# Optimization experiments

Measured on AMD Instinct MI355X. Metric: run time of the kernel, lower is better.

Reference implementation:

```python
import jax, jax.numpy as jnp
import numpy as np
from jax import lax

B, C, W = 16, 64, 125000  # batch, EEG channels, raw samples
KH, KW, SW, OC = 3, 2500, 1250, 32


def setup_inputs() -> dict:
    key = jax.random.key(0)
    ks = jax.random.split(key, 10)
    inp = {
        "x": jax.random.normal(ks[0], (B, 1, C, W), dtype=jnp.float32),
        # Conv2d(1->32, kernel=(3,2500))
        "conv_w": jax.random.normal(ks[1], (OC, 1, KH, KW), dtype=jnp.float32) * 0.02,
        "conv_b": jax.random.normal(ks[2], (OC,), dtype=jnp.float32) * 0.02,
        # Conv2d(32->1, kernel=(1,1))
        "conv2_w": jax.random.normal(ks[3], (1, OC, 1, 1), dtype=jnp.float32) * 0.1,
        "conv2_b": jax.random.normal(ks[4], (1,), dtype=jnp.float32) * 0.1,
        # nn.RNN(input_size=1, hidden_size=1): scalar weights
        "w_ih": jax.random.normal(ks[5], (1, 1), dtype=jnp.float32),
        "w_hh": jax.random.normal(ks[6], (1, 1), dtype=jnp.float32),
        "b_ih": jax.random.normal(ks[7], (1,), dtype=jnp.float32) * 0.1,
        "b_hh": jax.random.normal(ks[8], (1,), dtype=jnp.float32) * 0.1,
        # torch.rand(num_layers=1, B, 1) hidden init, reused for every row i
        "h0": jax.random.uniform(ks[9], (1, B, 1), dtype=jnp.float32),
    }
    return inp


def reference(x, conv_w, conv_b, conv2_w, conv2_b, w_ih, w_hh, b_ih, b_hh, h0):
    # F.pad(x, (0,0,1,1), 'replicate'): pad channel (height) dim by 1 each side
    xp = jnp.pad(x, ((0, 0), (0, 0), (1, 1), (0, 0)), mode="edge")
    # conv + relu -> [B, 32, C, T]
    y = lax.conv_general_dilated(
        xp, conv_w, window_strides=(1, SW), padding="VALID",
        dimension_numbers=("NCHW", "OIHW", "NCHW"))
    y = jax.nn.relu(y + conv_b[None, :, None, None])
    # 1x1 conv 32->1 + relu -> [B, C, T]
    z = jnp.einsum("bohw,o->bhw", y, conv2_w[0, :, 0, 0]) + conv2_b[0]
    z = jax.nn.relu(z)
    # Elman RNN with scalar weights, scanned over T; carry is [B, C]
    wih, whh = w_ih[0, 0], w_hh[0, 0]
    bias = b_ih[0] + b_hh[0]
    h_init = jnp.broadcast_to(h0[0, :, 0][:, None], z.shape[:2])  # [B, C]

    def step(h, xt):  # xt: [B, C]
        h = jnp.tanh(wih * xt + whh * h + bias)
        return h, None

    xs = jnp.moveaxis(z, -1, 0)  # [T, B, C]
    h_final, _ = lax.scan(step, h_init, xs)
    return jax.nn.sigmoid(h_final)  # [B, C]
```

## Files before the change

### kernel.cpp

```cpp
#include <hip/hip_runtime.h>
#include <math.h>

#define B_ 16
#define C_ 64
#define T_ 99
#define KW_ 1250
#define KP_ 1280
#define N_ 192
#define M_ (B_*C_*100)
#define BM 32
#define NCHUNK 40

typedef __attribute__((ext_vector_type(8))) _Float16 half8;
typedef __attribute__((ext_vector_type(2))) _Float16 half2_t;
typedef __attribute__((ext_vector_type(4))) float f32x4;
typedef __attribute__((ext_vector_type(2), aligned(8))) float f32x2;

__global__ __launch_bounds__(256) void wconv_kernel(const float* __restrict__ cw,
                                                    _Float16* __restrict__ wh)
{
    int n = blockIdx.x;
    int o = n / 6, rem = n - o * 6, kh = rem >> 1, hf = rem & 1;
    const float* src = cw + o * 7500 + kh * 2500 + hf * 1250;
    for (int k = threadIdx.x; k < KP_; k += 256)
        wh[n * KP_ + k] = (k < KW_) ? (_Float16)src[k] : (_Float16)0.f;
}

__global__ __launch_bounds__(256, 2) void gemm_kernel(const float* __restrict__ x,
                                                      const _Float16* __restrict__ wh,
                                                      _Float16* __restrict__ P)
{
    __shared__ __align__(16) _Float16 smA[BM * KP_];

    const int tid  = threadIdx.x;
    const int bt   = blockIdx.x;
    const int lane = tid & 63;
    const int wave = tid >> 6;
    const int wn   = wave * 48;
    const int l15  = lane & 15;
    const int lq   = lane >> 4;
    const int l4   = lane >> 2;
    const int lm4  = lane & 3;

    {
        const float* xb = x + (size_t)(bt * BM + wave * 8) * KW_;
#pragma unroll
        for (int rr = 0; rr < 8; rr++) {
            const int row = wave * 8 + rr;
            const float* xr = xb + (size_t)rr * KW_;
            _Float16* drow = smA + row * KP_;
            const int r7 = row & 7;
#pragma unroll
            for (int s = 0; s < 10; s++) {
                int c = s * 128 + lane * 2;
                f32x2 v = (c <= KW_ - 2) ? *(const f32x2*)(xr + c)
                                         : (f32x2){0.f, 0.f};
                int blk = (s * 16 + l4) ^ r7;
                *(half2_t*)(drow + blk * 8 + lm4 * 2) =
                    (half2_t){(_Float16)v.x, (_Float16)v.y};
            }
        }
    }
    __syncthreads();

    const _Float16* bbase = wh + (size_t)(wn + l15) * KP_ + lq * 8;

    f32x4 acc[2][3];
#pragma unroll
    for (int mi = 0; mi < 2; mi++)
#pragma unroll
        for (int ni = 0; ni < 3; ni++) acc[mi][ni] = (f32x4){0.f, 0.f, 0.f, 0.f};

#pragma unroll 4
    for (int ck = 0; ck < NCHUNK; ck++) {
        half8 bfr[3];
#pragma unroll
        for (int ni = 0; ni < 3; ni++)
            bfr[ni] = *(const half8*)(bbase + (size_t)ni * 16 * KP_ + ck * 32);
        half8 afr[2];
#pragma unroll
        for (int mi = 0; mi < 2; mi++) {
            int row = mi * 16 + l15;
            int blk = (ck * 4 + lq) ^ (row & 7);
            afr[mi] = *(const half8*)(smA + row * KP_ + blk * 8);
        }
#pragma unroll
        for (int mi = 0; mi < 2; mi++)
#pragma unroll
            for (int ni = 0; ni < 3; ni++)
                acc[mi][ni] = __builtin_amdgcn_mfma_f32_16x16x32_f16(
                    afr[mi], bfr[ni], acc[mi][ni], 0, 0, 0);
    }

#pragma unroll
    for (int mi = 0; mi < 2; mi++) {
#pragma unroll
        for (int r2 = 0; r2 < 4; r2++) {
            int rloc = mi * 16 + lq * 4 + r2;
            int xr   = bt * BM + rloc;
            int bc   = xr / 100;
            int j    = xr - bc * 100;
            size_t mp = ((size_t)(bc >> 6) * 100 + j) * 64 + (bc & 63);
#pragma unroll
            for (int ni = 0; ni < 3; ni++) {
                int n = wn + ni * 16 + l15;
                P[mp * N_ + n] = (_Float16)acc[mi][ni][r2];
            }
        }
    }
}

__global__ __launch_bounds__(256) void combine_kernel(const _Float16* __restrict__ P,
                                                      const float* __restrict__ conv_b,
                                                      const float* __restrict__ c2w,
                                                      const float* __restrict__ c2b,
                                                      float* __restrict__ z)
{
    __shared__ float Pl[64][193];
    __shared__ float red[4][64];
    const int t   = blockIdx.x;
    const int b   = blockIdx.y;
    const int tid = threadIdx.x;
    const int c   = tid & 63;
    const int og  = tid >> 6;

    float v[8];
#pragma unroll
    for (int o = 0; o < 8; o++) v[o] = conv_b[og * 8 + o];

    for (int hf = 0; hf < 2; hf++) {
        const int j = t + hf;
        const _Float16* Pb = P + (size_t)((b * 100 + j) * 64) * N_;
        __syncthreads();
#pragma unroll
        for (int i = 0; i < 6; i++) {
            int e   = i * 256 + tid;
            half8 hdat = *(const half8*)(Pb + e * 8);
            int row = e / 24;
            int col = (e - row * 24) * 8;
#pragma unroll
            for (int u = 0; u < 8; u++) Pl[row][col + u] = (float)hdat[u];
        }
        __syncthreads();
#pragma unroll
        for (int kh = 0; kh < 3; kh++) {
            int r = c + kh - 1;
            r = r < 0 ? 0 : (r > 63 ? 63 : r);
#pragma unroll
            for (int o = 0; o < 8; o++)
                v[o] += Pl[r][(og * 8 + o) * 6 + kh * 2 + hf];
        }
    }

    float part = 0.f;
#pragma unroll
    for (int o = 0; o < 8; o++) part += fmaxf(v[o], 0.f) * c2w[og * 8 + o];
    red[og][c] = part;
    __syncthreads();
    if (og == 0) {
        float zz = red[0][c] + red[1][c] + red[2][c] + red[3][c] + c2b[0];
        z[t * (B_ * C_) + b * 64 + c] = fmaxf(zz, 0.f);
    }
}

__global__ __launch_bounds__(256) void rnn_kernel(const float* __restrict__ z,
                                                  const float* __restrict__ w_ih,
                                                  const float* __restrict__ w_hh,
                                                  const float* __restrict__ b_ih,
                                                  const float* __restrict__ b_hh,
                                                  const float* __restrict__ h0,
                                                  float* __restrict__ out)
{
    __shared__ float zs[50][256];
    const int tid = threadIdx.x;
    const int g   = blockIdx.x * 256 + tid;
    const int b   = g >> 6;
    const float wih  = w_ih[0];
    const float whh  = w_hh[0];
    const float bias = b_ih[0] + b_hh[0];
    float h = h0[b];
    for (int t0 = 0; t0 < T_; t0 += 50) {
        const int nt = (T_ - t0) < 50 ? (T_ - t0) : 50;
        __syncthreads();
        for (int tt = 0; tt < nt; tt++)
            zs[tt][tid] = z[(t0 + tt) * (B_ * C_) + g];
        __syncthreads();
        for (int tt = 0; tt < nt; tt++)
            h = tanhf(fmaf(wih, zs[tt][tid], fmaf(whh, h, bias)));
    }
    out[g] = 1.f / (1.f + expf(-h));
}

extern "C" void kernel_launch(void* const* d_in, const int* in_sizes, int n_in,
                              void* d_out, int out_size, void* d_ws, size_t ws_size,
                              hipStream_t stream)
{
    const float* x   = (const float*)d_in[0];
    const float* cw  = (const float*)d_in[1];
    const float* cb  = (const float*)d_in[2];
    const float* c2w = (const float*)d_in[3];
    const float* c2b = (const float*)d_in[4];
    const float* wih = (const float*)d_in[5];
    const float* whh = (const float*)d_in[6];
    const float* bih = (const float*)d_in[7];
    const float* bhh = (const float*)d_in[8];
    const float* h0  = (const float*)d_in[9];
    float* out = (float*)d_out;

    const size_t whbytes = (size_t)N_ * KP_ * sizeof(_Float16);
    const size_t pbytes  = (size_t)M_ * N_ * sizeof(_Float16);
    const size_t zbytes  = (size_t)B_ * C_ * T_ * sizeof(float);

    if (ws_size < whbytes + pbytes + zbytes) return;

    _Float16* wh = (_Float16*)d_ws;
    _Float16* P  = (_Float16*)((char*)d_ws + whbytes);
    float*    z  = (float*)((char*)d_ws + whbytes + pbytes);

    wconv_kernel<<<N_, 256, 0, stream>>>(cw, wh);
    gemm_kernel<<<M_ / BM, 256, 0, stream>>>(x, wh, P);
    combine_kernel<<<dim3(T_, B_), 256, 0, stream>>>(P, cb, c2w, c2b, z);
    rnn_kernel<<<4, 256, 0, stream>>>(z, wih, whh, bih, bhh, h0, out);
}
```

Before: 874.9 us.

## Double-buffer GEMM A tiles via async global-to-LDS loads with 64-row blocks

The GEMM kernel no longer converts each block's whole 32x1280 input tile to fp16 in shared memory before computing. It now streams 128-column fp32 slices of a 64-row tile straight into a double-buffered LDS area using global_load_lds, with explicit waitcnt and barriers. The fp32-to-fp16 conversion happens in registers when fragments are built, and the tail past column 1250 is zeroed by masking. Waves are arranged 2x2 with 6 N-fragments each, so loading the raw input overlaps with the MFMA work and the B fragments are reused more. In exchange it reads a little past row ends, including past the end of x for the final row, relies on possibly unaligned 16-byte LDS loads, and needs more accumulator registers.

```diff
diff --git a/kernel.cpp b/kernel.cpp
--- a/kernel.cpp
+++ b/kernel.cpp
@@ -8,13 +8,15 @@
 #define KP_ 1280
 #define N_ 192
 #define M_ (B_*C_*100)
-#define BM 32
-#define NCHUNK 40
+#define BM 64
+#define NSC 10
 
 typedef __attribute__((ext_vector_type(8))) _Float16 half8;
-typedef __attribute__((ext_vector_type(2))) _Float16 half2_t;
 typedef __attribute__((ext_vector_type(4))) float f32x4;
-typedef __attribute__((ext_vector_type(2), aligned(8))) float f32x2;
+
+#define GLD_LDS16(gp, lp) \
+    __builtin_amdgcn_global_load_lds((const __attribute__((address_space(1))) void*)(gp), \
+                                     (__attribute__((address_space(3))) void*)(lp), 16, 0, 0)
 
 __global__ __launch_bounds__(256) void wconv_kernel(const float* __restrict__ cw,
                                                     _Float16* __restrict__ wh)
@@ -30,79 +32,110 @@
                                                       const _Float16* __restrict__ wh,
                                                       _Float16* __restrict__ P)
 {
-    __shared__ __align__(16) _Float16 smA[BM * KP_];
+    __shared__ __align__(16) float smA[2][BM * 128];
 
     const int tid  = threadIdx.x;
     const int bt   = blockIdx.x;
     const int lane = tid & 63;
     const int wave = tid >> 6;
-    const int wn   = wave * 48;
+    const int wm   = (wave & 1) * 32;
+    const int wn   = (wave >> 1) * 96;
     const int l15  = lane & 15;
     const int lq   = lane >> 4;
-    const int l4   = lane >> 2;
-    const int lm4  = lane & 3;
-
-    {
-        const float* xb = x + (size_t)(bt * BM + wave * 8) * KW_;
-#pragma unroll
-        for (int rr = 0; rr < 8; rr++) {
-            const int row = wave * 8 + rr;
-            const float* xr = xb + (size_t)rr * KW_;
-            _Float16* drow = smA + row * KP_;
-            const int r7 = row & 7;
-#pragma unroll
-            for (int s = 0; s < 10; s++) {
-                int c = s * 128 + lane * 2;
-                f32x2 v = (c <= KW_ - 2) ? *(const f32x2*)(xr + c)
-                                         : (f32x2){0.f, 0.f};
-                int blk = (s * 16 + l4) ^ r7;
-                *(half2_t*)(drow + blk * 8 + lm4 * 2) =
-                    (half2_t){(_Float16)v.x, (_Float16)v.y};
+
+    const int ls = lane >> 5;
+    const int lb = lane & 31;
+    const float* xbase = x + (size_t)bt * BM * KW_;
+
+#define STAGE(sc_, buf_) do {                                                    \
+        _Pragma("unroll") for (int i_ = 0; i_ < 8; i_++) {                       \
+            const int q_   = wave * 8 + i_;                                      \
+            const int row_ = 2 * q_ + ls;                                        \
+            const int g_   = lb ^ (row_ & 7);                                    \
+            GLD_LDS16(xbase + (size_t)row_ * KW_ + (sc_) * 128 + g_ * 4,         \
+                      &smA[buf_][q_ * 256]);                                     \
+        }                                                                        \
+    } while (0)
+
+    const _Float16* bbase = wh + (size_t)(wn + l15) * KP_ + lq * 8;
+
+    f32x4 acc[2][6];
+#pragma unroll
+    for (int mi = 0; mi < 2; mi++)
+#pragma unroll
+        for (int ni = 0; ni < 6; ni++) acc[mi][ni] = (f32x4){0.f, 0.f, 0.f, 0.f};
+
+    STAGE(0, 0);
+    STAGE(1, 1);
+
+    for (int sc = 0; sc < NSC; sc++) {
+        const int buf = sc & 1;
+        const float* Ab = &smA[buf][0];
+        const bool tail = (sc == NSC - 1);
+
+        if (sc < NSC - 1) asm volatile("s_waitcnt vmcnt(8)" ::: "memory");
+        else              asm volatile("s_waitcnt vmcnt(0)" ::: "memory");
+        __builtin_amdgcn_s_barrier();
+        __builtin_amdgcn_sched_barrier(0);
+
+#pragma unroll
+        for (int ckl = 0; ckl < 4; ckl++) {
+            const int ck = sc * 4 + ckl;
+            half8 bfr[6];
+#pragma unroll
+            for (int ni = 0; ni < 6; ni++)
+                bfr[ni] = *(const half8*)(bbase + (size_t)ni * 16 * KP_ + ck * 32);
+
+            half8 afr[2];
+#pragma unroll
+            for (int mi = 0; mi < 2; mi++) {
+                const int row = wm + mi * 16 + l15;
+                const int r7  = row & 7;
+                const int b0  = ckl * 8 + lq * 2;
+                f32x4 lo = *(const f32x4*)(Ab + row * 128 + ((b0    ) ^ r7) * 4);
+                f32x4 hi = *(const f32x4*)(Ab + row * 128 + ((b0 + 1) ^ r7) * 4);
+                if (tail && ckl == 3) {
+                    if (lq != 0) {
+                        lo = (f32x4){0.f, 0.f, 0.f, 0.f};
+                        hi = (f32x4){0.f, 0.f, 0.f, 0.f};
+                    } else {
+                        lo[2] = 0.f; lo[3] = 0.f;
+                        hi = (f32x4){0.f, 0.f, 0.f, 0.f};
+                    }
+                }
+                half8 a;
+                a[0] = (_Float16)lo[0]; a[1] = (_Float16)lo[1];
+                a[2] = (_Float16)lo[2]; a[3] = (_Float16)lo[3];
+                a[4] = (_Float16)hi[0]; a[5] = (_Float16)hi[1];
+                a[6] = (_Float16)hi[2]; a[7] = (_Float16)hi[3];
+                afr[mi] = a;
             }
-        }
-    }
-    __syncthreads();
-
-    const _Float16* bbase = wh + (size_t)(wn + l15) * KP_ + lq * 8;
-
-    f32x4 acc[2][3];
-#pragma unroll
-    for (int mi = 0; mi < 2; mi++)
-#pragma unroll
-        for (int ni = 0; ni < 3; ni++) acc[mi][ni] = (f32x4){0.f, 0.f, 0.f, 0.f};
-
-#pragma unroll 4
-    for (int ck = 0; ck < NCHUNK; ck++) {
-        half8 bfr[3];
-#pragma unroll
-        for (int ni = 0; ni < 3; ni++)
-            bfr[ni] = *(const half8*)(bbase + (size_t)ni * 16 * KP_ + ck * 32);
-        half8 afr[2];
-#pragma unroll
-        for (int mi = 0; mi < 2; mi++) {
-            int row = mi * 16 + l15;
-            int blk = (ck * 4 + lq) ^ (row & 7);
-            afr[mi] = *(const half8*)(smA + row * KP_ + blk * 8);
-        }
-#pragma unroll
-        for (int mi = 0; mi < 2; mi++)
-#pragma unroll
-            for (int ni = 0; ni < 3; ni++)
-                acc[mi][ni] = __builtin_amdgcn_mfma_f32_16x16x32_f16(
-                    afr[mi], bfr[ni], acc[mi][ni], 0, 0, 0);
-    }
+#pragma unroll
+            for (int mi = 0; mi < 2; mi++)
+#pragma unroll
+                for (int ni = 0; ni < 6; ni++)
+                    acc[mi][ni] = __builtin_amdgcn_mfma_f32_16x16x32_f16(
+                        afr[mi], bfr[ni], acc[mi][ni], 0, 0, 0);
+        }
+
+        asm volatile("s_waitcnt lgkmcnt(0)" ::: "memory");
+        __builtin_amdgcn_s_barrier();
+        __builtin_amdgcn_sched_barrier(0);
+        if (sc + 2 < NSC) STAGE(sc + 2, buf);
+    }
+#undef STAGE
 
 #pragma unroll
     for (int mi = 0; mi < 2; mi++) {
 #pragma unroll
         for (int r2 = 0; r2 < 4; r2++) {
-            int rloc = mi * 16 + lq * 4 + r2;
+            int rloc = wm + mi * 16 + lq * 4 + r2;
             int xr   = bt * BM + rloc;
             int bc   = xr / 100;
             int j    = xr - bc * 100;
             size_t mp = ((size_t)(bc >> 6) * 100 + j) * 64 + (bc & 63);
 #pragma unroll
-            for (int ni = 0; ni < 3; ni++) {
+            for (int ni = 0; ni < 6; ni++) {
                 int n = wn + ni * 16 + l15;
                 P[mp * N_ + n] = (_Float16)acc[mi][ni][r2];
             }
```

Measured after the change: 834.7 us. 4.6% less time.
